# Performance work log

Hardware: AMD Instinct MI355X
Metric: run time of the kernel (lower is better)

The kernel has to match this reference:

```python
import jax, jax.numpy as jnp
import numpy as np

NUM_HEADS = 16
D_MODEL = 1024
DEPTH = D_MODEL // NUM_HEADS
THRESHOLD = 0.1
BATCH = 2
SEQ = 2048


def setup_inputs() -> dict:
    key = jax.random.key(0)
    ks = jax.random.split(key, 9)
    w_scale = 1.0 / np.sqrt(D_MODEL)
    Q = jax.random.normal(ks[0], (BATCH, SEQ, D_MODEL), dtype=jnp.float32)
    T = jax.random.normal(ks[1], (BATCH, SEQ, D_MODEL), dtype=jnp.float32)
    V = jax.random.normal(ks[2], (BATCH, SEQ, D_MODEL), dtype=jnp.float32)
    Wq = jax.random.normal(ks[3], (NUM_HEADS, D_MODEL, DEPTH), dtype=jnp.float32) * w_scale
    Wk = jax.random.normal(ks[4], (NUM_HEADS, D_MODEL, DEPTH), dtype=jnp.float32) * w_scale
    Wv = jax.random.normal(ks[5], (NUM_HEADS, D_MODEL, DEPTH), dtype=jnp.float32) * w_scale
    Wo = jax.random.normal(ks[6], (D_MODEL, D_MODEL), dtype=jnp.float32) * w_scale
    bq = jnp.zeros((NUM_HEADS, DEPTH), dtype=jnp.float32)
    bk = jnp.zeros((NUM_HEADS, DEPTH), dtype=jnp.float32)
    bv = jnp.zeros((NUM_HEADS, DEPTH), dtype=jnp.float32)
    bo = jnp.zeros((D_MODEL,), dtype=jnp.float32)
    return {"Q": Q, "T": T, "V": V, "Wq": Wq, "bq": bq, "Wk": Wk, "bk": bk,
            "Wv": Wv, "bv": bv, "Wo": Wo, "bo": bo}


def reference(Q, T, V, Wq, bq, Wk, bk, Wv, bv, Wo, bo):
    # Per-head projections (stacked over heads): [B,S,D] x [H,D,E] -> [B,H,S,E]
    q = jnp.einsum('bsd,hde->bhse', Q, Wq) + bq[None, :, None, :]
    k = jnp.einsum('bsd,hde->bhse', T, Wk) + bk[None, :, None, :]
    v = jnp.einsum('bsd,hde->bhse', V, Wv) + bv[None, :, None, :]

    # Raw scores (NOT pre-scaled): [B,H,S,S]
    scores = jnp.einsum('bhqe,bhke->bhqk', q, k)
    # tf.where(A>thr, A, -2**32 * cast(A>thr)) -> failing entries become 0
    scores = jnp.where(scores > THRESHOLD, scores, jnp.zeros((), scores.dtype))
    # M = 1 - lower_band(ones): +1 on strictly upper-triangular entries
    seq = scores.shape[-1]
    upper = jnp.triu(jnp.ones((seq, seq), dtype=scores.dtype), k=1)
    scores = (scores + upper) / jnp.sqrt(jnp.asarray(DEPTH, scores.dtype))

    attn = jax.nn.softmax(scores, axis=-1)
    out = jnp.einsum('bhqk,bhke->bhqe', attn, v)  # [B,H,S,E]
    B, H, S, E = out.shape
    concat = out.transpose(0, 2, 1, 3).reshape(B, S, H * E)  # [B,S,D]
    return concat @ Wo + bo
```

## Files before the change

### kernel.cpp

```cpp
#include <hip/hip_runtime.h>
#include <stdint.h>


typedef __attribute__((ext_vector_type(8))) short bf16x8;
typedef __attribute__((ext_vector_type(4))) float f32x4;

#define DEVFN static __device__ __forceinline__

static constexpr int S_ = 2048;
static constexpr int H_ = 16;

DEVFN unsigned short f2bf(float x) {
  union { float f; uint32_t u; } v; v.f = x;
  const uint32_t r = v.u + 0x7fffu + ((v.u >> 16) & 1u);
  return (unsigned short)(r >> 16);
}

DEVFN f32x4 fzero() { f32x4 v = {0.f, 0.f, 0.f, 0.f}; return v; }

DEVFN void gld_lds16(const void* g, void* lds) {
  __builtin_amdgcn_global_load_lds(
      (const __attribute__((address_space(1))) void*)g,
      (__attribute__((address_space(3))) void*)lds, 16, 0, 0);
}

__global__ void prep_weights(const float* __restrict__ Wq, const float* __restrict__ Wk,
                             const float* __restrict__ Wv, const float* __restrict__ Wo,
                             unsigned short* __restrict__ dstBase) {
  const int z = blockIdx.z;
  const float* src = (z == 0) ? Wq : (z == 1) ? Wk : (z == 2) ? Wv : Wo;
  unsigned short* dst = dstBase + (size_t)z * (1024u * 1024u);
  const int idx = blockIdx.x * 256 + threadIdx.x;
  const int c = idx & 1023;
  const int d0 = (idx >> 10) << 3;
  unsigned short hv[8];
#pragma unroll
  for (int t = 0; t < 8; ++t) {
    const int d = d0 + t;
    const float v = (z < 3) ? src[(size_t)((c >> 6) * 1024 + d) * 64 + (c & 63)]
                            : src[(size_t)d * 1024 + c];
    hv[t] = f2bf(v);
  }
  *(uint4*)(dst + (size_t)c * 1024 + d0) = *(const uint4*)hv;
}

__global__ void convert_a(const float* __restrict__ Qm, const float* __restrict__ Tm,
                          const float* __restrict__ Vm, unsigned short* __restrict__ aq,
                          unsigned short* __restrict__ at2, unsigned short* __restrict__ av) {
  const int z = blockIdx.z;
  const float* s = (z == 0) ? Qm : (z == 1) ? Tm : Vm;
  unsigned short* d = (z == 0) ? aq : (z == 1) ? at2 : av;
  const size_t i = ((size_t)blockIdx.x * 256 + threadIdx.x) * 8;
  const float4 f0 = *(const float4*)(s + i);
  const float4 f1 = *(const float4*)(s + i + 4);
  uint32_t d0, d1, d2, d3;
  asm("v_cvt_pk_bf16_f32 %0, %1, %2" : "=v"(d0) : "v"(f0.x), "v"(f0.y));
  asm("v_cvt_pk_bf16_f32 %0, %1, %2" : "=v"(d1) : "v"(f0.z), "v"(f0.w));
  asm("v_cvt_pk_bf16_f32 %0, %1, %2" : "=v"(d2) : "v"(f1.x), "v"(f1.y));
  asm("v_cvt_pk_bf16_f32 %0, %1, %2" : "=v"(d3) : "v"(f1.z), "v"(f1.w));
  uint4 o; o.x = d0; o.y = d1; o.z = d2; o.w = d3;
  *(uint4*)(d + i) = o;
}

__global__ __launch_bounds__(256, 4)
void proj_gemm(const unsigned short* __restrict__ Aq,
               const unsigned short* __restrict__ At2,
               const unsigned short* __restrict__ Av,
               const unsigned short* __restrict__ Wt,
               const float* __restrict__ bq, const float* __restrict__ bk,
               const float* __restrict__ bv, unsigned short* __restrict__ qb,
               unsigned short* __restrict__ kb, unsigned short* __restrict__ vtb) {
  __shared__ unsigned short At[2][128 * 32];
  __shared__ unsigned short Bt[2][128 * 32];

  const int tid = threadIdx.x;
  const int lane = tid & 63;
  const int w = tid >> 6;
  const int g = lane >> 4, c = lane & 15;
  const int wm = w >> 1, wn = w & 1;

  const int m0 = blockIdx.x * 128;
  const int proj = blockIdx.y >> 3;
  const int n0 = (blockIdx.y & 7) * 128;

  const unsigned short* Abf = (proj == 0) ? Aq : (proj == 1) ? At2 : Av;
  const unsigned short* W = Wt + (size_t)proj * (1024u * 1024u);

  f32x4 acc[4][4];
#pragma unroll
  for (int i = 0; i < 4; ++i)
#pragma unroll
    for (int j = 0; j < 4; ++j) acc[i][j] = fzero();

  const int srow = lane >> 2;
  const int sch = lane & 3;

  auto stage = [&](int kt, int buf) {
#pragma unroll
    for (int u = 0; u < 2; ++u) {
      const int row = u * 64 + w * 16 + srow;
      const int ch = sch ^ ((row >> 1) & 3);
      gld_lds16(Abf + (size_t)(m0 + row) * 1024 + kt * 32 + ch * 8,
                &At[buf][(u * 64 + w * 16) * 32]);
      gld_lds16(W + (size_t)(n0 + row) * 1024 + kt * 32 + ch * 8,
                &Bt[buf][(u * 64 + w * 16) * 32]);
    }
  };

  stage(0, 0);
  __syncthreads();

  for (int kt = 0; kt < 32; ++kt) {
    const int buf = kt & 1;
    if (kt < 31) stage(kt + 1, buf ^ 1);

    bf16x8 af[4], bfr[4];
#pragma unroll
    for (int mi = 0; mi < 4; ++mi) {
      const int row = wm * 64 + mi * 16 + c;
      af[mi] = *(const bf16x8*)&At[buf][row * 32 + ((g ^ ((row >> 1) & 3))) * 8];
    }
#pragma unroll
    for (int ni = 0; ni < 4; ++ni) {
      const int row = wn * 64 + ni * 16 + c;
      bfr[ni] = *(const bf16x8*)&Bt[buf][row * 32 + ((g ^ ((row >> 1) & 3))) * 8];
    }
#pragma unroll
    for (int mi = 0; mi < 4; ++mi)
#pragma unroll
      for (int ni = 0; ni < 4; ++ni)
        acc[mi][ni] = __builtin_amdgcn_mfma_f32_16x16x32_bf16(af[mi], bfr[ni],
                                                              acc[mi][ni], 0, 0, 0);
    __syncthreads();
  }

  const float* bias = (proj == 0) ? bq : (proj == 1) ? bk : bv;
  if (proj < 2) {
    unsigned short* dptr = (proj == 0) ? qb : kb;
#pragma unroll
    for (int ni = 0; ni < 4; ++ni) {
      const int colb = n0 + wn * 64 + ni * 16 + c;
      const float bc = bias[colb];
      const int hh = colb >> 6, e = colb & 63;
#pragma unroll
      for (int mi = 0; mi < 4; ++mi)
#pragma unroll
        for (int r = 0; r < 4; ++r) {
          const int row = m0 + wm * 64 + mi * 16 + g * 4 + r;
          const int bb = row >> 11, s = row & 2047;
          dptr[(((size_t)(bb * H_ + hh)) * S_ + s) * 64 + e] = f2bf(acc[mi][ni][r] + bc);
        }
    }
  } else {
#pragma unroll
    for (int ni = 0; ni < 4; ++ni) {
      const int colb = n0 + wn * 64 + ni * 16 + c;
      const float bc = bias[colb];
      const int hh = colb >> 6, e = colb & 63;
#pragma unroll
      for (int mi = 0; mi < 4; ++mi) {
        const int rowb = m0 + wm * 64 + mi * 16 + g * 4;
        const int bb = rowb >> 11, s0 = rowb & 2047;
        const float v0 = acc[mi][ni][0] + bc, v1 = acc[mi][ni][1] + bc;
        const float v2 = acc[mi][ni][2] + bc, v3 = acc[mi][ni][3] + bc;
        uint2 pk;
        asm("v_cvt_pk_bf16_f32 %0, %1, %2" : "=v"(pk.x) : "v"(v0), "v"(v1));
        asm("v_cvt_pk_bf16_f32 %0, %1, %2" : "=v"(pk.y) : "v"(v2), "v"(v3));
        *(uint2*)&vtb[(((size_t)(bb * H_ + hh)) * 64 + e) * S_ + s0] = pk;
      }
    }
  }
}

__global__ __launch_bounds__(256, 4)
void attn_kernel(const unsigned short* __restrict__ qb,
                 const unsigned short* __restrict__ kb,
                 const unsigned short* __restrict__ vtb,
                 unsigned short* __restrict__ att) {
  __shared__ unsigned short Kt[2][64 * 64];
  __shared__ unsigned short Vt[2][64 * 64];
  __shared__ unsigned short Pt[4][16 * 64];

  const int tid = threadIdx.x;
  const int lane = tid & 63;
  const int w = tid >> 6;
  const int g = lane >> 4, c = lane & 15;

  const int orig = blockIdx.x;
  const int logical = ((orig & 7) << 7) | (orig >> 3);
  const int qblk = logical & 31;
  const int bh = logical >> 5;
  const int hh = bh & 15, bz = bh >> 4;

  const int q0w = qblk * 64 + w * 16;
  const unsigned short* qh = qb + (size_t)bh * S_ * 64;
  const unsigned short* kh = kb + (size_t)bh * S_ * 64;
  const unsigned short* vh = vtb + (size_t)bh * 64 * S_;

  bf16x8 aq[2];
#pragma unroll
  for (int t = 0; t < 2; ++t)
    aq[t] = *(const bf16x8*)&qh[(size_t)(q0w + c) * 64 + t * 32 + g * 8];

  bf16x8 onesB;
#pragma unroll
  for (int i = 0; i < 8; ++i) onesB[i] = (short)0x3F80;

  f32x4 O[4];
  f32x4 accL;
#pragma unroll
  for (int ne = 0; ne < 4; ++ne) O[ne] = fzero();
  accL = fzero();

  constexpr float L2E = 1.4426950408889634f;
  const float S2 = 0.125f * L2E;
  const float B2 = 0.125f * L2E;
  const int iq = q0w + c;

  int kaOff[2][4], bvOff[2][4], paOff[2], pwOff[4];
#pragma unroll
  for (int ks = 0; ks < 2; ++ks) {
#pragma unroll
    for (int mi = 0; mi < 4; ++mi) {
      const int row = mi * 16 + c;
      kaOff[ks][mi] = 2 * (row * 64 + ((ks * 4 + g) ^ (row & 7)) * 8);
    }
#pragma unroll
    for (int ne = 0; ne < 4; ++ne) {
      const int e = ne * 16 + c;
      bvOff[ks][ne] = 2 * (e * 64 + ((ks * 4 + g) ^ (e & 7)) * 8);
    }
    paOff[ks] = 2 * (c * 64 + ((ks * 4 + g) ^ (c & 7)) * 8);
  }
#pragma unroll
  for (int mi = 0; mi < 4; ++mi)
    pwOff[mi] = 2 * (c * 64 + ((2 * mi + (g >> 1)) ^ (c & 7)) * 8 + (g & 1) * 4);

  const int srow = w * 8 + (lane >> 3);
  const int sch = (lane & 7) ^ (srow & 7);
  const unsigned short* kS0 = kh + (size_t)srow * 64 + sch * 8;
  const unsigned short* kS1 = kh + (size_t)(32 + srow) * 64 + sch * 8;
  const unsigned short* vS0 = vh + (size_t)srow * S_ + sch * 8;
  const unsigned short* vS1 = vh + (size_t)(32 + srow) * S_ + sch * 8;

  {
    gld_lds16(kS0, &Kt[0][(w * 8) * 64]);
    gld_lds16(kS1, &Kt[0][(32 + w * 8) * 64]);
    gld_lds16(vS0, &Vt[0][(w * 8) * 64]);
    gld_lds16(vS1, &Vt[0][(32 + w * 8) * 64]);
  }
  __syncthreads();

#define ATTN_BODY(JT, CUR)                                                     \
  do {                                                                         \
    const int j0 = (JT) * 64;                                                  \
    if ((JT) < 31) {             \
      gld_lds16(kS0 + 4096, &Kt[CUR ^ 1][(w * 8) * 64]);                       \
      gld_lds16(kS1 + 4096, &Kt[CUR ^ 1][(32 + w * 8) * 64]);                  \
      gld_lds16(vS0 + 64, &Vt[CUR ^ 1][(w * 8) * 64]);                         \
      gld_lds16(vS1 + 64, &Vt[CUR ^ 1][(32 + w * 8) * 64]);                    \
      kS0 += 4096; kS1 += 4096; vS0 += 64; vS1 += 64;                          \
    }                                                                          \
    f32x4 sa[4];                                                               \
    _Pragma("unroll")                                                          \
    for (int mi = 0; mi < 4; ++mi) sa[mi] = fzero();                           \
    __builtin_amdgcn_s_setprio(1);                                             \
    _Pragma("unroll")                                                          \
    for (int ks = 0; ks < 2; ++ks)                                             \
      _Pragma("unroll")                                                        \
      for (int mi = 0; mi < 4; ++mi) {                                         \
        const bf16x8 ka =                                                      \
            *(const bf16x8*)((const char*)&Kt[CUR][0] + kaOff[ks][mi]);        \
        sa[mi] = __builtin_amdgcn_mfma_f32_16x16x32_bf16(ka, aq[ks], sa[mi],   \
                                                         0, 0, 0);             \
      }                                                                        \
    __builtin_amdgcn_s_setprio(0);                                             \
    const bool allUp = (j0 >= q0w + 16);                                       \
    const bool noneUp = (j0 + 63 <= q0w);                                      \
    _Pragma("unroll")                                                          \
    for (int mi = 0; mi < 4; ++mi) {                                           \
      float pv[4];                                                             \
      if (allUp || noneUp) {                                                   \
        const float bb = allUp ? B2 : 0.f;                                     \
        _Pragma("unroll")                                                      \
        for (int r = 0; r < 4; ++r) {                                          \
          const float v = sa[mi][r];                                           \
          pv[r] = __builtin_amdgcn_exp2f((v > 0.1f)                            \
                                             ? __builtin_fmaf(v, S2, bb)      \
                                             : bb);                            \
        }                                                                      \
      } else {                                                                 \
        _Pragma("unroll")                                                      \
        for (int r = 0; r < 4; ++r) {                                          \
          const float v = sa[mi][r];                                           \
          const float bb = (j0 + mi * 16 + g * 4 + r > iq) ? B2 : 0.f;         \
          pv[r] = __builtin_amdgcn_exp2f((v > 0.1f)                            \
                                             ? __builtin_fmaf(v, S2, bb)      \
                                             : bb);                           \
        }                                                                      \
      }                                                                        \
      uint2 d;                                                                 \
      asm("v_cvt_pk_bf16_f32 %0, %1, %2" : "=v"(d.x) : "v"(pv[0]), "v"(pv[1]));\
      asm("v_cvt_pk_bf16_f32 %0, %1, %2" : "=v"(d.y) : "v"(pv[2]), "v"(pv[3]));\
      *(uint2*)((char*)&Pt[w][0] + pwOff[mi]) = d;                             \
    }                                                                          \
    asm volatile("s_waitcnt lgkmcnt(0)" ::: "memory");                         \
    __builtin_amdgcn_sched_barrier(0);                                         \
    __builtin_amdgcn_s_setprio(1);                                             \
    _Pragma("unroll")                                                          \
    for (int ks = 0; ks < 2; ++ks) {                                           \
      const bf16x8 pa =                                                        \
          *(const bf16x8*)((const char*)&Pt[w][0] + paOff[ks]);                \
      accL = __builtin_amdgcn_mfma_f32_16x16x32_bf16(pa, onesB, accL, 0, 0, 0);\
      _Pragma("unroll")                                                        \
      for (int ne = 0; ne < 4; ++ne) {                                         \
        const bf16x8 bv8 =                                                     \
            *(const bf16x8*)((const char*)&Vt[CUR][0] + bvOff[ks][ne]);        \
        O[ne] = __builtin_amdgcn_mfma_f32_16x16x32_bf16(pa, bv8, O[ne],        \
                                                        0, 0, 0);              \
      }                                                                        \
    }                                                                          \
    __builtin_amdgcn_s_setprio(0);                                             \
    __syncthreads();                                                           \
  } while (0)

  for (int jt = 0; jt < 32; jt += 2) {
    ATTN_BODY(jt, 0);
    ATTN_BODY(jt + 1, 1);
  }
#undef ATTN_BODY

#pragma unroll
  for (int r = 0; r < 4; ++r) {
    const float il = 1.f / accL[r];
    const int qg = q0w + g * 4 + r;
    const size_t ro = ((size_t)(bz * S_ + qg)) * 1024 + hh * 64;
#pragma unroll
    for (int ne = 0; ne < 4; ++ne)
      att[ro + ne * 16 + c] = f2bf(O[ne][r] * il);
  }
}

__global__ __launch_bounds__(256, 3)
void out_gemm(const unsigned short* __restrict__ att,
              const unsigned short* __restrict__ WoT,
              const float* __restrict__ bo, float* __restrict__ outp) {
  __shared__ unsigned short At[2][128 * 32];
  __shared__ unsigned short Bt[2][128 * 32];

  const int tid = threadIdx.x;
  const int lane = tid & 63;
  const int w = tid >> 6;
  const int g = lane >> 4, c = lane & 15;
  const int wm = w >> 1, wn = w & 1;
  const int m0 = blockIdx.x * 128;
  const int n0 = blockIdx.y * 128;

  f32x4 acc[4][4];
#pragma unroll
  for (int i = 0; i < 4; ++i)
#pragma unroll
    for (int j = 0; j < 4; ++j) acc[i][j] = fzero();

  const int srow = lane >> 2;
  const int sch = lane & 3;

  auto stage = [&](int kt, int buf) {
#pragma unroll
    for (int u = 0; u < 2; ++u) {
      const int row = u * 64 + w * 16 + srow;
      const int ch = sch ^ ((row >> 1) & 3);
      gld_lds16(att + (size_t)(m0 + row) * 1024 + kt * 32 + ch * 8,
                &At[buf][(u * 64 + w * 16) * 32]);
      gld_lds16(WoT + (size_t)(n0 + row) * 1024 + kt * 32 + ch * 8,
                &Bt[buf][(u * 64 + w * 16) * 32]);
    }
  };

  stage(0, 0);
  __syncthreads();

  for (int kt = 0; kt < 32; ++kt) {
    const int buf = kt & 1;
    if (kt < 31) stage(kt + 1, buf ^ 1);

    bf16x8 af[4], bfr[4];
#pragma unroll
    for (int mi = 0; mi < 4; ++mi) {
      const int row = wm * 64 + mi * 16 + c;
      af[mi] = *(const bf16x8*)&At[buf][row * 32 + ((g ^ ((row >> 1) & 3))) * 8];
    }
#pragma unroll
    for (int ni = 0; ni < 4; ++ni) {
      const int row = wn * 64 + ni * 16 + c;
      bfr[ni] = *(const bf16x8*)&Bt[buf][row * 32 + ((g ^ ((row >> 1) & 3))) * 8];
    }
#pragma unroll
    for (int mi = 0; mi < 4; ++mi)
#pragma unroll
      for (int ni = 0; ni < 4; ++ni)
        acc[mi][ni] = __builtin_amdgcn_mfma_f32_16x16x32_bf16(af[mi], bfr[ni],
                                                              acc[mi][ni], 0, 0, 0);
    __syncthreads();
  }

#pragma unroll
  for (int ni = 0; ni < 4; ++ni) {
    const int colb = n0 + wn * 64 + ni * 16 + c;
    const float bc = bo[colb];
#pragma unroll
    for (int mi = 0; mi < 4; ++mi)
#pragma unroll
      for (int r = 0; r < 4; ++r) {
        const int row = m0 + wm * 64 + mi * 16 + g * 4 + r;
        outp[(size_t)row * 1024 + colb] = acc[mi][ni][r] + bc;
      }
  }
}

extern "C" void kernel_launch(void* const* d_in, const int* in_sizes, int n_in,
                              void* d_out, int out_size, void* d_ws, size_t ws_size,
                              hipStream_t stream) {
  const float* Q  = (const float*)d_in[0];
  const float* T  = (const float*)d_in[1];
  const float* V  = (const float*)d_in[2];
  const float* Wq = (const float*)d_in[3];
  const float* bq = (const float*)d_in[4];
  const float* Wk = (const float*)d_in[5];
  const float* bk = (const float*)d_in[6];
  const float* Wv = (const float*)d_in[7];
  const float* bv = (const float*)d_in[8];
  const float* Wo = (const float*)d_in[9];
  const float* bo = (const float*)d_in[10];

  const size_t MB = 1024ull * 1024ull;
  if (ws_size < 40 * MB) return;

  uint8_t* ws = (uint8_t*)d_ws;
  unsigned short* Wt  = (unsigned short*)(ws);
  unsigned short* qb  = (unsigned short*)(ws + 8 * MB);
  unsigned short* kb  = (unsigned short*)(ws + 16 * MB);
  unsigned short* vtb = (unsigned short*)(ws + 24 * MB);
  unsigned short* attb = (unsigned short*)(ws + 32 * MB);

  unsigned short* aQ = (unsigned short*)d_out;
  unsigned short* aT = aQ + 4ull * 1024ull * 1024ull;
  unsigned short* aV = attb;

  prep_weights<<<dim3(512, 1, 4), 256, 0, stream>>>(Wq, Wk, Wv, Wo, Wt);
  convert_a<<<dim3(2048, 1, 3), 256, 0, stream>>>(Q, T, V, aQ, aT, aV);
  proj_gemm<<<dim3(32, 24), 256, 0, stream>>>(aQ, aT, aV, Wt, bq, bk, bv,
                                              qb, kb, vtb);
  attn_kernel<<<dim3(1024), 256, 0, stream>>>(qb, kb, vtb, attb);
  out_gemm<<<dim3(32, 8), 256, 0, stream>>>(attb, Wt + 3ull * 1024ull * 1024ull,
                                            bo, (float*)d_out);
}
```

Measured before the change: 138.1 us.

## Fuse fp32-to-bf16 input conversion into projection GEMM and double attention rows per wave

Drops the separate convert_a kernel: proj_gemm now loads fp32 activations straight into LDS with a swizzled layout and converts them to bf16 in registers before the MFMA. Separately, the attention kernel gives each wave 32 query rows instead of 16, so every K/V fragment read from LDS feeds two MFMAs, and the grid is halved to 512 blocks. This removes a full read/write pass over the inputs and cuts LDS traffic per MFMA. In exchange it doubles the fp32 A-tile LDS footprint and global load volume in the GEMM, and lowers occupancy in both kernels through the launch bounds and the larger accumulator state.

```diff
diff --git a/kernel.cpp b/kernel.cpp
--- a/kernel.cpp
+++ b/kernel.cpp
@@ -17,6 +17,8 @@
 }
 
 DEVFN f32x4 fzero() { f32x4 v = {0.f, 0.f, 0.f, 0.f}; return v; }
+
+union U8 { uint32_t u[4]; bf16x8 v; };
 
 DEVFN void gld_lds16(const void* g, void* lds) {
   __builtin_amdgcn_global_load_lds(
@@ -44,33 +46,13 @@
   *(uint4*)(dst + (size_t)c * 1024 + d0) = *(const uint4*)hv;
 }
 
-__global__ void convert_a(const float* __restrict__ Qm, const float* __restrict__ Tm,
-                          const float* __restrict__ Vm, unsigned short* __restrict__ aq,
-                          unsigned short* __restrict__ at2, unsigned short* __restrict__ av) {
-  const int z = blockIdx.z;
-  const float* s = (z == 0) ? Qm : (z == 1) ? Tm : Vm;
-  unsigned short* d = (z == 0) ? aq : (z == 1) ? at2 : av;
-  const size_t i = ((size_t)blockIdx.x * 256 + threadIdx.x) * 8;
-  const float4 f0 = *(const float4*)(s + i);
-  const float4 f1 = *(const float4*)(s + i + 4);
-  uint32_t d0, d1, d2, d3;
-  asm("v_cvt_pk_bf16_f32 %0, %1, %2" : "=v"(d0) : "v"(f0.x), "v"(f0.y));
-  asm("v_cvt_pk_bf16_f32 %0, %1, %2" : "=v"(d1) : "v"(f0.z), "v"(f0.w));
-  asm("v_cvt_pk_bf16_f32 %0, %1, %2" : "=v"(d2) : "v"(f1.x), "v"(f1.y));
-  asm("v_cvt_pk_bf16_f32 %0, %1, %2" : "=v"(d3) : "v"(f1.z), "v"(f1.w));
-  uint4 o; o.x = d0; o.y = d1; o.z = d2; o.w = d3;
-  *(uint4*)(d + i) = o;
-}
-
-__global__ __launch_bounds__(256, 4)
-void proj_gemm(const unsigned short* __restrict__ Aq,
-               const unsigned short* __restrict__ At2,
-               const unsigned short* __restrict__ Av,
-               const unsigned short* __restrict__ Wt,
+__global__ __launch_bounds__(256, 3)
+void proj_gemm(const float* __restrict__ Qm, const float* __restrict__ Tm,
+               const float* __restrict__ Vm, const unsigned short* __restrict__ Wt,
                const float* __restrict__ bq, const float* __restrict__ bk,
                const float* __restrict__ bv, unsigned short* __restrict__ qb,
                unsigned short* __restrict__ kb, unsigned short* __restrict__ vtb) {
-  __shared__ unsigned short At[2][128 * 32];
+  __shared__ float Af[2][128 * 32];
   __shared__ unsigned short Bt[2][128 * 32];
 
   const int tid = threadIdx.x;
@@ -83,7 +65,7 @@
   const int proj = blockIdx.y >> 3;
   const int n0 = (blockIdx.y & 7) * 128;
 
-  const unsigned short* Abf = (proj == 0) ? Aq : (proj == 1) ? At2 : Av;
+  const float* Asrc = (proj == 0) ? Qm : (proj == 1) ? Tm : Vm;
   const unsigned short* W = Wt + (size_t)proj * (1024u * 1024u);
 
   f32x4 acc[4][4];
@@ -92,16 +74,23 @@
 #pragma unroll
     for (int j = 0; j < 4; ++j) acc[i][j] = fzero();
 
-  const int srow = lane >> 2;
-  const int sch = lane & 3;
+  const int arow = w * 8 + (lane >> 3);
+  const int ach = lane & 7;
+  const int brow = w * 16 + (lane >> 2);
+  const int bch = lane & 3;
 
   auto stage = [&](int kt, int buf) {
 #pragma unroll
+    for (int u = 0; u < 4; ++u) {
+      const int row = u * 32 + arow;
+      const int ch = ach ^ (row & 7);
+      gld_lds16(Asrc + (size_t)(m0 + row) * 1024 + kt * 32 + ch * 4,
+                &Af[buf][(u * 32 + w * 8) * 32]);
+    }
+#pragma unroll
     for (int u = 0; u < 2; ++u) {
-      const int row = u * 64 + w * 16 + srow;
-      const int ch = sch ^ ((row >> 1) & 3);
-      gld_lds16(Abf + (size_t)(m0 + row) * 1024 + kt * 32 + ch * 8,
-                &At[buf][(u * 64 + w * 16) * 32]);
+      const int row = u * 64 + brow;
+      const int ch = bch ^ ((row >> 1) & 3);
       gld_lds16(W + (size_t)(n0 + row) * 1024 + kt * 32 + ch * 8,
                 &Bt[buf][(u * 64 + w * 16) * 32]);
     }
@@ -118,7 +107,15 @@
 #pragma unroll
     for (int mi = 0; mi < 4; ++mi) {
       const int row = wm * 64 + mi * 16 + c;
-      af[mi] = *(const bf16x8*)&At[buf][row * 32 + ((g ^ ((row >> 1) & 3))) * 8];
+      const int swz = row & 7;
+      const float4 fa = *(const float4*)&Af[buf][row * 32 + ((2 * g) ^ swz) * 4];
+      const float4 fb = *(const float4*)&Af[buf][row * 32 + ((2 * g + 1) ^ swz) * 4];
+      U8 u8;
+      asm("v_cvt_pk_bf16_f32 %0, %1, %2" : "=v"(u8.u[0]) : "v"(fa.x), "v"(fa.y));
+      asm("v_cvt_pk_bf16_f32 %0, %1, %2" : "=v"(u8.u[1]) : "v"(fa.z), "v"(fa.w));
+      asm("v_cvt_pk_bf16_f32 %0, %1, %2" : "=v"(u8.u[2]) : "v"(fb.x), "v"(fb.y));
+      asm("v_cvt_pk_bf16_f32 %0, %1, %2" : "=v"(u8.u[3]) : "v"(fb.z), "v"(fb.w));
+      af[mi] = u8.v;
     }
 #pragma unroll
     for (int ni = 0; ni < 4; ++ni) {
@@ -172,14 +169,14 @@
   }
 }
 
-__global__ __launch_bounds__(256, 4)
+__global__ __launch_bounds__(256, 2)
 void attn_kernel(const unsigned short* __restrict__ qb,
                  const unsigned short* __restrict__ kb,
                  const unsigned short* __restrict__ vtb,
                  unsigned short* __restrict__ att) {
   __shared__ unsigned short Kt[2][64 * 64];
   __shared__ unsigned short Vt[2][64 * 64];
-  __shared__ unsigned short Pt[4][16 * 64];
+  __shared__ unsigned short Pt[4][32 * 64];
 
   const int tid = threadIdx.x;
   const int lane = tid & 63;
@@ -187,54 +184,58 @@
   const int g = lane >> 4, c = lane & 15;
 
   const int orig = blockIdx.x;
-  const int logical = ((orig & 7) << 7) | (orig >> 3);
-  const int qblk = logical & 31;
-  const int bh = logical >> 5;
+  const int logical = ((orig & 7) << 6) | (orig >> 3);
+  const int qblk = logical & 15;
+  const int bh = logical >> 4;
   const int hh = bh & 15, bz = bh >> 4;
 
-  const int q0w = qblk * 64 + w * 16;
+  const int q0w = qblk * 128 + w * 32;
   const unsigned short* qh = qb + (size_t)bh * S_ * 64;
   const unsigned short* kh = kb + (size_t)bh * S_ * 64;
   const unsigned short* vh = vtb + (size_t)bh * 64 * S_;
 
-  bf16x8 aq[2];
-#pragma unroll
-  for (int t = 0; t < 2; ++t)
-    aq[t] = *(const bf16x8*)&qh[(size_t)(q0w + c) * 64 + t * 32 + g * 8];
+  bf16x8 aq[2][2];
+#pragma unroll
+  for (int m = 0; m < 2; ++m)
+#pragma unroll
+    for (int t = 0; t < 2; ++t)
+      aq[m][t] = *(const bf16x8*)&qh[(size_t)(q0w + m * 16 + c) * 64 + t * 32 + g * 8];
 
   bf16x8 onesB;
 #pragma unroll
   for (int i = 0; i < 8; ++i) onesB[i] = (short)0x3F80;
 
-  f32x4 O[4];
-  f32x4 accL;
-#pragma unroll
-  for (int ne = 0; ne < 4; ++ne) O[ne] = fzero();
-  accL = fzero();
+  f32x4 O[2][4];
+  f32x4 accL[2];
+#pragma unroll
+  for (int m = 0; m < 2; ++m) {
+#pragma unroll
+    for (int ne = 0; ne < 4; ++ne) O[m][ne] = fzero();
+    accL[m] = fzero();
+  }
 
   constexpr float L2E = 1.4426950408889634f;
   const float S2 = 0.125f * L2E;
   const float B2 = 0.125f * L2E;
-  const int iq = q0w + c;
-
-  int kaOff[2][4], bvOff[2][4], paOff[2], pwOff[4];
+
+  int kvOff[2][4], paOff[2][2], pwOff[2][4];
 #pragma unroll
   for (int ks = 0; ks < 2; ++ks) {
 #pragma unroll
     for (int mi = 0; mi < 4; ++mi) {
       const int row = mi * 16 + c;
-      kaOff[ks][mi] = 2 * (row * 64 + ((ks * 4 + g) ^ (row & 7)) * 8);
-    }
-#pragma unroll
-    for (int ne = 0; ne < 4; ++ne) {
-      const int e = ne * 16 + c;
-      bvOff[ks][ne] = 2 * (e * 64 + ((ks * 4 + g) ^ (e & 7)) * 8);
-    }
-    paOff[ks] = 2 * (c * 64 + ((ks * 4 + g) ^ (c & 7)) * 8);
-  }
-#pragma unroll
-  for (int mi = 0; mi < 4; ++mi)
-    pwOff[mi] = 2 * (c * 64 + ((2 * mi + (g >> 1)) ^ (c & 7)) * 8 + (g & 1) * 4);
+      kvOff[ks][mi] = 2 * (row * 64 + ((ks * 4 + g) ^ (row & 7)) * 8);
+    }
+#pragma unroll
+    for (int m = 0; m < 2; ++m)
+      paOff[m][ks] = 2 * ((m * 16 + c) * 64 + ((ks * 4 + g) ^ (c & 7)) * 8);
+  }
+#pragma unroll
+  for (int m = 0; m < 2; ++m)
+#pragma unroll
+    for (int mi = 0; mi < 4; ++mi)
+      pwOff[m][mi] =
+          2 * ((m * 16 + c) * 64 + ((2 * mi + (g >> 1)) ^ (c & 7)) * 8 + (g & 1) * 4);
 
   const int srow = w * 8 + (lane >> 3);
   const int sch = (lane & 7) ^ (srow & 7);
@@ -261,63 +262,78 @@
       gld_lds16(vS1 + 64, &Vt[CUR ^ 1][(32 + w * 8) * 64]);                    \
       kS0 += 4096; kS1 += 4096; vS0 += 64; vS1 += 64;                          \
     }                                                                          \
-    f32x4 sa[4];                                                               \
+    f32x4 sa[2][4];                                                            \
     _Pragma("unroll")                                                          \
-    for (int mi = 0; mi < 4; ++mi) sa[mi] = fzero();                           \
+    for (int m = 0; m < 2; ++m)                                                \
+      _Pragma("unroll")                                                        \
+      for (int mi = 0; mi < 4; ++mi) sa[m][mi] = fzero();                      \
     __builtin_amdgcn_s_setprio(1);                                             \
     _Pragma("unroll")                                                          \
     for (int ks = 0; ks < 2; ++ks)                                             \
       _Pragma("unroll")                                                        \
       for (int mi = 0; mi < 4; ++mi) {                                         \
         const bf16x8 ka =                                                      \
-            *(const bf16x8*)((const char*)&Kt[CUR][0] + kaOff[ks][mi]);        \
-        sa[mi] = __builtin_amdgcn_mfma_f32_16x16x32_bf16(ka, aq[ks], sa[mi],   \
-                                                         0, 0, 0);             \
+            *(const bf16x8*)((const char*)&Kt[CUR][0] + kvOff[ks][mi]);        \
+        sa[0][mi] = __builtin_amdgcn_mfma_f32_16x16x32_bf16(ka, aq[0][ks],     \
+                                                            sa[0][mi], 0, 0, 0);\
+        sa[1][mi] = __builtin_amdgcn_mfma_f32_16x16x32_bf16(ka, aq[1][ks],     \
+                                                            sa[1][mi], 0, 0, 0);\
       }                                                                        \
     __builtin_amdgcn_s_setprio(0);                                             \
-    const bool allUp = (j0 >= q0w + 16);                                       \
+    const bool allUp = (j0 >= q0w + 32);                                       \
     const bool noneUp = (j0 + 63 <= q0w);                                      \
     _Pragma("unroll")                                                          \
-    for (int mi = 0; mi < 4; ++mi) {                                           \
-      float pv[4];                                                             \
-      if (allUp || noneUp) {                                                   \
-        const float bb = allUp ? B2 : 0.f;                                     \
-        _Pragma("unroll")                                                      \
-        for (int r = 0; r < 4; ++r) {                                          \
-          const float v = sa[mi][r];                                           \
-          pv[r] = __builtin_amdgcn_exp2f((v > 0.1f)                            \
-                                             ? __builtin_fmaf(v, S2, bb)      \
-                                             : bb);                            \
+    for (int m = 0; m < 2; ++m) {                                              \
+      const int iq = q0w + m * 16 + c;                                         \
+      _Pragma("unroll")                                                        \
+      for (int mi = 0; mi < 4; ++mi) {                                         \
+        float pv[4];                                                           \
+        if (allUp || noneUp) {                                                 \
+          const float bb = allUp ? B2 : 0.f;                                   \
+          _Pragma("unroll")                                                    \
+          for (int r = 0; r < 4; ++r) {                                        \
+            const float v = sa[m][mi][r];                                      \
+            pv[r] = __builtin_amdgcn_exp2f(                                    \
+                (v > 0.1f) ? __builtin_fmaf(v, S2, bb) : bb);                  \
+          }                                                                    \
+        } else {                                                               \
+          _Pragma("unroll")                                                    \
+          for (int r = 0; r < 4; ++r) {                                        \
+            const float v = sa[m][mi][r];                                      \
+            const float bb = (j0 + mi * 16 + g * 4 + r > iq) ? B2 : 0.f;       \
+            pv[r] = __builtin_amdgcn_exp2f(                                    \
+                (v > 0.1f) ? __builtin_fmaf(v, S2, bb) : bb);                  \
+          }                                                                    \
         }                                                                      \
-      } else {                                                                 \
-        _Pragma("unroll")                                                      \
-        for (int r = 0; r < 4; ++r) {                                          \
-          const float v = sa[mi][r];                                           \
-          const float bb = (j0 + mi * 16 + g * 4 + r > iq) ? B2 : 0.f;         \
-          pv[r] = __builtin_amdgcn_exp2f((v > 0.1f)                            \
-                                             ? __builtin_fmaf(v, S2, bb)      \
-                                             : bb);                           \
-        }                                                                      \
+        uint2 d;                                                               \
+        asm("v_cvt_pk_bf16_f32 %0, %1, %2"                                     \
+            : "=v"(d.x) : "v"(pv[0]), "v"(pv[1]));                             \
+        asm("v_cvt_pk_bf16_f32 %0, %1, %2"                                     \
+            : "=v"(d.y) : "v"(pv[2]), "v"(pv[3]));                             \
+        *(uint2*)((char*)&Pt[w][0] + pwOff[m][mi]) = d;                        \
       }                                                                        \
-      uint2 d;                                                                 \
-      asm("v_cvt_pk_bf16_f32 %0, %1, %2" : "=v"(d.x) : "v"(pv[0]), "v"(pv[1]));\
-      asm("v_cvt_pk_bf16_f32 %0, %1, %2" : "=v"(d.y) : "v"(pv[2]), "v"(pv[3]));\
-      *(uint2*)((char*)&Pt[w][0] + pwOff[mi]) = d;                             \
     }                                                                          \
     asm volatile("s_waitcnt lgkmcnt(0)" ::: "memory");                         \
     __builtin_amdgcn_sched_barrier(0);                                         \
     __builtin_amdgcn_s_setprio(1);                                             \
     _Pragma("unroll")                                                          \
     for (int ks = 0; ks < 2; ++ks) {                                           \
-      const bf16x8 pa =                                                        \
-          *(const bf16x8*)((const char*)&Pt[w][0] + paOff[ks]);                \
-      accL = __builtin_amdgcn_mfma_f32_16x16x32_bf16(pa, onesB, accL, 0, 0, 0);\
+      const bf16x8 pa0 =                                                       \
+          *(const bf16x8*)((const char*)&Pt[w][0] + paOff[0][ks]);             \
+      const bf16x8 pa1 =                                                       \
+          *(const bf16x8*)((const char*)&Pt[w][0] + paOff[1][ks]);             \
+      accL[0] = __builtin_amdgcn_mfma_f32_16x16x32_bf16(pa0, onesB, accL[0],   \
+                                                        0, 0, 0);              \
+      accL[1] = __builtin_amdgcn_mfma_f32_16x16x32_bf16(pa1, onesB, accL[1],   \
+                                                        0, 0, 0);              \
       _Pragma("unroll")                                                        \
       for (int ne = 0; ne < 4; ++ne) {                                         \
         const bf16x8 bv8 =                                                     \
-            *(const bf16x8*)((const char*)&Vt[CUR][0] + bvOff[ks][ne]);        \
-        O[ne] = __builtin_amdgcn_mfma_f32_16x16x32_bf16(pa, bv8, O[ne],        \
-                                                        0, 0, 0);              \
+            *(const bf16x8*)((const char*)&Vt[CUR][0] + kvOff[ks][ne]);        \
+        O[0][ne] = __builtin_amdgcn_mfma_f32_16x16x32_bf16(pa0, bv8, O[0][ne], \
+                                                           0, 0, 0);           \
+        O[1][ne] = __builtin_amdgcn_mfma_f32_16x16x32_bf16(pa1, bv8, O[1][ne], \
+                                                           0, 0, 0);           \
       }                                                                        \
     }                                                                          \
     __builtin_amdgcn_s_setprio(0);                                             \
@@ -331,14 +347,16 @@
 #undef ATTN_BODY
 
 #pragma unroll
-  for (int r = 0; r < 4; ++r) {
-    const float il = 1.f / accL[r];
-    const int qg = q0w + g * 4 + r;
-    const size_t ro = ((size_t)(bz * S_ + qg)) * 1024 + hh * 64;
-#pragma unroll
-    for (int ne = 0; ne < 4; ++ne)
-      att[ro + ne * 16 + c] = f2bf(O[ne][r] * il);
-  }
+  for (int m = 0; m < 2; ++m)
+#pragma unroll
+    for (int r = 0; r < 4; ++r) {
+      const float il = 1.f / accL[m][r];
+      const int qg = q0w + m * 16 + g * 4 + r;
+      const size_t ro = ((size_t)(bz * S_ + qg)) * 1024 + hh * 64;
+#pragma unroll
+      for (int ne = 0; ne < 4; ++ne)
+        att[ro + ne * 16 + c] = f2bf(O[m][ne][r] * il);
+    }
 }
 
 __global__ __launch_bounds__(256, 3)
@@ -443,15 +461,10 @@
   unsigned short* vtb = (unsigned short*)(ws + 24 * MB);
   unsigned short* attb = (unsigned short*)(ws + 32 * MB);
 
-  unsigned short* aQ = (unsigned short*)d_out;
-  unsigned short* aT = aQ + 4ull * 1024ull * 1024ull;
-  unsigned short* aV = attb;
-
   prep_weights<<<dim3(512, 1, 4), 256, 0, stream>>>(Wq, Wk, Wv, Wo, Wt);
-  convert_a<<<dim3(2048, 1, 3), 256, 0, stream>>>(Q, T, V, aQ, aT, aV);
-  proj_gemm<<<dim3(32, 24), 256, 0, stream>>>(aQ, aT, aV, Wt, bq, bk, bv,
+  proj_gemm<<<dim3(32, 24), 256, 0, stream>>>(Q, T, V, Wt, bq, bk, bv,
                                               qb, kb, vtb);
-  attn_kernel<<<dim3(1024), 256, 0, stream>>>(qb, kb, vtb, attb);
+  attn_kernel<<<dim3(512), 256, 0, stream>>>(qb, kb, vtb, attb);
   out_gemm<<<dim3(32, 8), 256, 0, stream>>>(attb, Wt + 3ull * 1024ull * 1024ull,
                                             bo, (float*)d_out);
 }
```

Measured after the change: 133.1 us. 1.04x faster.
